# Performance work log

Hardware: AMD Instinct MI355X
Metric: run time of the kernel (lower is better)

Reference implementation:

```python
import jax, jax.numpy as jnp
import numpy as np

N = 50000
E = 600000
D_IN = 128
HID = 128
OUT = 64


def setup_inputs() -> dict:
    key = jax.random.key(0)
    ks = jax.random.split(key, 12)
    x = jax.random.normal(ks[0], (N, D_IN), dtype=jnp.float32)
    edge_index = jax.random.randint(ks[1], (2, E), 0, N, dtype=jnp.int32)
    def lin(k, fan_in, fan_out):
        lim = 1.0 / np.sqrt(fan_in)
        kw, kb = jax.random.split(k)
        W = jax.random.uniform(kw, (fan_in, fan_out), minval=-lim, maxval=lim, dtype=jnp.float32)
        b = jax.random.uniform(kb, (fan_out,), minval=-lim, maxval=lim, dtype=jnp.float32)
        return W, b
    W1, b1 = lin(ks[2], D_IN, HID)
    W2, b2 = lin(ks[3], HID, HID)
    W3, b3 = lin(ks[4], HID, HID)
    fcW, fcb = lin(ks[5], HID, OUT)
    return {"x": x, "edge_index": edge_index, "W1": W1, "b1": b1,
            "W2": W2, "b2": b2, "W3": W3, "b3": b3, "fcW": fcW, "fcb": fcb}


def _gcn_prep(edge_index):
    # add self loops, compute symmetric normalization deg^-1/2 * deg^-1/2
    loop = jnp.arange(N, dtype=edge_index.dtype)
    src = jnp.concatenate([edge_index[0], loop])
    dst = jnp.concatenate([edge_index[1], loop])
    deg = jax.ops.segment_sum(jnp.ones_like(dst, dtype=jnp.float32), dst, num_segments=N)
    dinv = jnp.where(deg > 0, jax.lax.rsqrt(deg), 0.0)
    norm = dinv[src] * dinv[dst]  # [E+N]
    return src, dst, norm


def _gcn_layer(x, src, dst, norm, W, b):
    h = x @ W                      # [N, F_out]
    msg = h[src] * norm[:, None]   # gather + scale, [E+N, F_out]
    agg = jax.ops.segment_sum(msg, dst, num_segments=N)
    return agg + b


def reference(x, edge_index, W1, b1, W2, b2, W3, b3, fcW, fcb):
    src, dst, norm = _gcn_prep(edge_index)
    x = jax.nn.relu(_gcn_layer(x, src, dst, norm, W1, b1))
    x = jax.nn.relu(_gcn_layer(x, src, dst, norm, W2, b2))
    x = jax.nn.relu(_gcn_layer(x, src, dst, norm, W3, b3))
    virtual_node_embedding = x[-1]  # last node's embedding [HID]
    out = virtual_node_embedding @ fcW + fcb  # [OUT]
    return out
```

## Files before the change

### kernel.cpp

```cpp
#include <hip/hip_runtime.h>

#define NF 128
#define OUTF 64

#define M2 1
#define M1 2
#define M0 4

#define CAP_F2 2048
#define CAP_E3 4096
#define CAP_F1 32768
#define CAP_E2 65536
#define CAP_F0 131072
#define CAP_E1 262144


__global__ void k_seed(int* __restrict__ mark, int* __restrict__ F2,
                       int* __restrict__ cnt, int last) {
    if (threadIdx.x == 0) {
        mark[last] = M2;
        F2[0] = last;
        cnt[0] = 1;
    }
}

__global__ void k_mark(const int* __restrict__ src, const int* __restrict__ dst, int E,
                       int* __restrict__ mark, int checkBit, int setBit, int last,
                       int2* __restrict__ Elist, int Ecap, int* __restrict__ eCnt,
                       int* __restrict__ Flist, int Fcap, int* __restrict__ fCnt,
                       const int* __restrict__ selfList, const int* __restrict__ selfCnt,
                       int selfCap)
{
    int i = blockIdx.x * blockDim.x + threadIdx.x;

    if (selfList) {
        int sc = *selfCnt; if (sc > selfCap) sc = selfCap;
        if (i < sc) {
            int v = selfList[i];
            if (!(atomicOr(&mark[v], setBit) & setBit)) {
                int p = atomicAdd(fCnt, 1);
                if (p < Fcap) Flist[p] = v;
            }
        }
    }
    if (i < E) {
        int d = dst[i];
        bool hit = checkBit ? ((mark[d] & checkBit) != 0) : (d == last);
        if (hit) {
            int s = src[i];
            int p = atomicAdd(eCnt, 1);
            if (p < Ecap) Elist[p] = make_int2(s, d);
            if (!(atomicOr(&mark[s], setBit) & setBit)) {
                int q = atomicAdd(fCnt, 1);
                if (q < Fcap) Flist[q] = s;
            }
        }
    }
}

__global__ void k_degm(const int* __restrict__ dst, const int* __restrict__ mark,
                       int* __restrict__ deg, int E) {
    int i = blockIdx.x * blockDim.x + threadIdx.x;
    if (i < E) {
        int d = dst[i];
        if (mark[d]) atomicAdd(&deg[d], 1);
    }
}

__global__ void k_dinvm(const int* __restrict__ mark, const int* __restrict__ deg,
                        float* __restrict__ dinv, int n) {
    int i = blockIdx.x * blockDim.x + threadIdx.x;
    if (i < n && mark[i]) dinv[i] = rsqrtf(1.0f + (float)deg[i]);
}

__global__ __launch_bounds__(256) void k_gemm_rows(
    const int* __restrict__ list, const int* __restrict__ cntPtr, int cap,
    const float* __restrict__ Xin, const float* __restrict__ bias,
    const float* __restrict__ W, const float* __restrict__ dinv,
    const int* __restrict__ mark, int aggBit, int last,
    float* __restrict__ H, float* __restrict__ AGG)
{
    __shared__ float wsm[128][128];
    const int t = threadIdx.x;

    {
        const float4* W4 = (const float4*)W;
        float4* S4 = (float4*)&wsm[0][0];
        #pragma unroll
        for (int it = 0; it < 16; ++it) S4[it * 256 + t] = W4[it * 256 + t];
    }
    __syncthreads();

    int cnt = *cntPtr; if (cnt > cap) cnt = cap;
    const int wave = t >> 6, lane = t & 63;

    for (int base = blockIdx.x * 4; base < cnt; base += gridDim.x * 4) {
        int r = base + wave;
        if (r >= cnt) continue;
        int v = list[r];
        size_t off = (size_t)v * NF;

        float x0, x1;
        if (bias) {
            x0 = fmaxf(Xin[off + lane]      + bias[lane],      0.f);
            x1 = fmaxf(Xin[off + lane + 64] + bias[lane + 64], 0.f);
        } else {
            x0 = Xin[off + lane];
            x1 = Xin[off + lane + 64];
        }

        float a0 = 0.f, a1 = 0.f;
        #pragma unroll 16
        for (int k = 0; k < 64; ++k) {
            float xk = __shfl(x0, k);
            a0 += xk * wsm[k][lane];
            a1 += xk * wsm[k][lane + 64];
        }
        #pragma unroll 16
        for (int k = 0; k < 64; ++k) {
            float xk = __shfl(x1, k);
            a0 += xk * wsm[k + 64][lane];
            a1 += xk * wsm[k + 64][lane + 64];
        }

        H[off + lane]      = a0;
        H[off + lane + 64] = a1;

        bool doAgg = (mark ? ((mark[v] & aggBit) != 0) : false) || (v == last);
        if (doAgg) {
            float di = dinv[v], s2 = di * di;
            AGG[off + lane]      = a0 * s2;
            AGG[off + lane + 64] = a1 * s2;
        }
    }
}

__global__ void k_scat(const int2* __restrict__ list, const int* __restrict__ cntPtr, int cap,
                       const float* __restrict__ dinv, const float* __restrict__ H,
                       float* __restrict__ AGG)
{
    int cnt = *cntPtr; if (cnt > cap) cnt = cap;
    int t = threadIdx.x;
    for (int i = blockIdx.x; i < cnt; i += gridDim.x) {
        int2 e = list[i];
        float w = dinv[e.x] * dinv[e.y];
        atomicAdd(&AGG[(size_t)e.y * NF + t], H[(size_t)e.x * NF + t] * w);
    }
}

__global__ void k_fc(const float* __restrict__ AGG3, const float* __restrict__ b3,
                     const float* __restrict__ fcW, const float* __restrict__ fcb,
                     float* __restrict__ out, int last)
{
    __shared__ float xrow[NF];
    int j = threadIdx.x;
    size_t off = (size_t)last * NF;
    xrow[j]      = fmaxf(AGG3[off + j]      + b3[j],      0.f);
    xrow[j + 64] = fmaxf(AGG3[off + j + 64] + b3[j + 64], 0.f);
    __syncthreads();
    float acc = fcb[j];
    #pragma unroll 16
    for (int k = 0; k < NF; ++k) acc += xrow[k] * fcW[k * OUTF + j];
    out[j] = acc;
}

extern "C" void kernel_launch(void* const* d_in, const int* in_sizes, int n_in,
                              void* d_out, int out_size, void* d_ws, size_t ws_size,
                              hipStream_t stream)
{
    const float* x    = (const float*)d_in[0];
    const int*   ei   = (const int*)d_in[1];
    const float* W1   = (const float*)d_in[2];
    const float* b1   = (const float*)d_in[3];
    const float* W2   = (const float*)d_in[4];
    const float* b2   = (const float*)d_in[5];
    const float* W3   = (const float*)d_in[6];
    const float* b3   = (const float*)d_in[7];
    const float* fcW  = (const float*)d_in[8];
    const float* fcb  = (const float*)d_in[9];
    float* out = (float*)d_out;

    const int n = in_sizes[0] / NF;
    const int E = in_sizes[1] / 2;
    const int* src = ei;
    const int* dst = ei + E;
    const int last = n - 1;

    char* wp = (char*)d_ws;
    auto alloc = [&](size_t bytes) -> void* {
        void* r = (void*)wp;
        wp += (bytes + 255) & ~(size_t)255;
        return r;
    };
    int*   deg  = (int*)alloc((size_t)n * 4);
    int*   mark = (int*)alloc((size_t)n * 4);
    int*   cnt  = (int*)alloc(64 * 4);
    size_t zbytes = (char*)wp - (char*)deg;

    float* dinv = (float*)alloc((size_t)n * 4);
    int*   F2   = (int*) alloc(CAP_F2 * 4);
    int2*  E3   = (int2*)alloc(CAP_E3 * 8);
    int*   F1   = (int*) alloc(CAP_F1 * 4);
    int2*  E2   = (int2*)alloc(CAP_E2 * 8);
    int*   F0   = (int*) alloc(CAP_F0 * 4);
    int2*  E1   = (int2*)alloc(CAP_E1 * 8);
    float* H    = (float*)alloc((size_t)n * NF * 4);
    float* aggA = (float*)alloc((size_t)n * NF * 4);
    float* aggB = (float*)alloc((size_t)n * NF * 4);

    const int B  = 256;
    const int EB = (E + B - 1) / B;
    const int NB = (n + B - 1) / B;

    hipMemsetAsync(deg, 0, zbytes, stream);
    k_seed<<<1, 64, 0, stream>>>(mark, F2, cnt, last);

    k_mark<<<EB, B, 0, stream>>>(src, dst, E, mark, 0,  M2, last,
                                 E3, CAP_E3, &cnt[1], F2, CAP_F2, &cnt[0],
                                 nullptr, nullptr, 0);
    k_mark<<<EB, B, 0, stream>>>(src, dst, E, mark, M2, M1, last,
                                 E2, CAP_E2, &cnt[3], F1, CAP_F1, &cnt[2],
                                 F2, &cnt[0], CAP_F2);
    k_mark<<<EB, B, 0, stream>>>(src, dst, E, mark, M1, M0, last,
                                 E1, CAP_E1, &cnt[5], F0, CAP_F0, &cnt[4],
                                 F1, &cnt[2], CAP_F1);

    k_degm <<<EB, B, 0, stream>>>(dst, mark, deg, E);
    k_dinvm<<<NB, B, 0, stream>>>(mark, deg, dinv, n);

    k_gemm_rows<<<384, B, 0, stream>>>(F0, &cnt[4], CAP_F0, x, nullptr, W1,
                                       dinv, mark, M1, -1, H, aggA);
    k_scat<<<2048, 128, 0, stream>>>(E1, &cnt[5], CAP_E1, dinv, H, aggA);

    k_gemm_rows<<<384, B, 0, stream>>>(F1, &cnt[2], CAP_F1, aggA, b1, W2,
                                       dinv, mark, M2, -1, H, aggB);
    k_scat<<<2048, 128, 0, stream>>>(E2, &cnt[3], CAP_E2, dinv, H, aggB);

    k_gemm_rows<<<384, B, 0, stream>>>(F2, &cnt[0], CAP_F2, aggB, b2, W3,
                                       dinv, nullptr, 0, last, H, aggA);
    k_scat<<<2048, 128, 0, stream>>>(E3, &cnt[1], CAP_E3, dinv, H, aggA);

    k_fc<<<1, 64, 0, stream>>>(aggA, b3, fcW, fcb, out, last);
}
```

Measured before the change: 167.8 us.

## Restructure GCN pipeline: dense layer-1 GEMM, fused edge scan, single-block tail

Drops the third frontier-marking pass and runs the layer-1 GEMM over every node, then scatters layer-1 messages by scanning the full edge list with a block-local queue. Degree counting moves into the first mark pass, and dinv is recomputed inline instead of stored. Layers 2 and 3 plus the final FC are fused into one single-block kernel to remove launch overhead. The trade-off is more layer-1 work (all rows instead of the 2-hop frontier) and serial layer-2/3 processing on a single workgroup, which could be slow if frontiers are large.

```diff
diff --git a/kernel.cpp b/kernel.cpp
--- a/kernel.cpp
+++ b/kernel.cpp
@@ -5,110 +5,89 @@
 
 #define M2 1
 #define M1 2
-#define M0 4
-
-#define CAP_F2 2048
-#define CAP_E3 4096
-#define CAP_F1 32768
-#define CAP_E2 65536
-#define CAP_F0 131072
-#define CAP_E1 262144
-
-
-__global__ void k_seed(int* __restrict__ mark, int* __restrict__ F2,
-                       int* __restrict__ cnt, int last) {
-    if (threadIdx.x == 0) {
-        mark[last] = M2;
-        F2[0] = last;
-        cnt[0] = 1;
-    }
-}
-
-__global__ void k_mark(const int* __restrict__ src, const int* __restrict__ dst, int E,
-                       int* __restrict__ mark, int checkBit, int setBit, int last,
-                       int2* __restrict__ Elist, int Ecap, int* __restrict__ eCnt,
-                       int* __restrict__ Flist, int Fcap, int* __restrict__ fCnt,
-                       const int* __restrict__ selfList, const int* __restrict__ selfCnt,
-                       int selfCap)
+
+#define CAP_F2 4096
+#define CAP_E3 8192
+#define CAP_F1 65536
+#define CAP_E2 131072
+
+
+__device__ __forceinline__ float dinv_of(const int* deg, int v) {
+    return rsqrtf(1.0f + (float)deg[v]);
+}
+
+__global__ void k_mark1(const int* __restrict__ src, const int* __restrict__ dst, int E,
+                        int last, int* __restrict__ deg, int* __restrict__ mark,
+                        int* __restrict__ cnt, int2* __restrict__ E3l, int* __restrict__ F2)
 {
     int i = blockIdx.x * blockDim.x + threadIdx.x;
-
-    if (selfList) {
-        int sc = *selfCnt; if (sc > selfCap) sc = selfCap;
-        if (i < sc) {
-            int v = selfList[i];
-            if (!(atomicOr(&mark[v], setBit) & setBit)) {
-                int p = atomicAdd(fCnt, 1);
-                if (p < Fcap) Flist[p] = v;
-            }
-        }
-    }
-    if (i < E) {
-        int d = dst[i];
-        bool hit = checkBit ? ((mark[d] & checkBit) != 0) : (d == last);
-        if (hit) {
-            int s = src[i];
-            int p = atomicAdd(eCnt, 1);
-            if (p < Ecap) Elist[p] = make_int2(s, d);
-            if (!(atomicOr(&mark[s], setBit) & setBit)) {
-                int q = atomicAdd(fCnt, 1);
-                if (q < Fcap) Flist[q] = s;
-            }
-        }
-    }
-}
-
-__global__ void k_degm(const int* __restrict__ dst, const int* __restrict__ mark,
-                       int* __restrict__ deg, int E) {
+    if (i == 0) {
+        if (!(atomicOr(&mark[last], M2) & M2)) {
+            int q = atomicAdd(&cnt[0], 1);
+            if (q < CAP_F2) F2[q] = last;
+        }
+    }
+    if (i >= E) return;
+    int d = dst[i];
+    atomicAdd(&deg[d], 1);
+    if (d == last) {
+        int s = src[i];
+        int pe = atomicAdd(&cnt[1], 1);
+        if (pe < CAP_E3) E3l[pe] = make_int2(s, d);
+        if (!(atomicOr(&mark[s], M2) & M2)) {
+            int q = atomicAdd(&cnt[0], 1);
+            if (q < CAP_F2) F2[q] = s;
+        }
+    }
+}
+
+__global__ void k_mark2(const int* __restrict__ src, const int* __restrict__ dst, int E,
+                        int* __restrict__ mark, int* __restrict__ cnt,
+                        const int* __restrict__ F2, int* __restrict__ F1,
+                        int2* __restrict__ E2l)
+{
     int i = blockIdx.x * blockDim.x + threadIdx.x;
-    if (i < E) {
-        int d = dst[i];
-        if (mark[d]) atomicAdd(&deg[d], 1);
-    }
-}
-
-__global__ void k_dinvm(const int* __restrict__ mark, const int* __restrict__ deg,
-                        float* __restrict__ dinv, int n) {
-    int i = blockIdx.x * blockDim.x + threadIdx.x;
-    if (i < n && mark[i]) dinv[i] = rsqrtf(1.0f + (float)deg[i]);
-}
-
-__global__ __launch_bounds__(256) void k_gemm_rows(
-    const int* __restrict__ list, const int* __restrict__ cntPtr, int cap,
-    const float* __restrict__ Xin, const float* __restrict__ bias,
-    const float* __restrict__ W, const float* __restrict__ dinv,
-    const int* __restrict__ mark, int aggBit, int last,
-    float* __restrict__ H, float* __restrict__ AGG)
+    int cF2 = cnt[0]; if (cF2 > CAP_F2) cF2 = CAP_F2;
+    if (i < cF2) {
+        int v = F2[i];
+        if (!(atomicOr(&mark[v], M1) & M1)) {
+            int q = atomicAdd(&cnt[2], 1);
+            if (q < CAP_F1) F1[q] = v;
+        }
+    }
+    if (i >= E) return;
+    int d = dst[i];
+    if (mark[d] & M2) {
+        int s = src[i];
+        int pe = atomicAdd(&cnt[3], 1);
+        if (pe < CAP_E2) E2l[pe] = make_int2(s, d);
+        if (!(atomicOr(&mark[s], M1) & M1)) {
+            int q = atomicAdd(&cnt[2], 1);
+            if (q < CAP_F1) F1[q] = s;
+        }
+    }
+}
+
+__global__ __launch_bounds__(256) void k_gemm1(
+    const float* __restrict__ X, const float* __restrict__ W1,
+    const int* __restrict__ mark, const int* __restrict__ deg,
+    float* __restrict__ H, float* __restrict__ agg1, int n)
 {
     __shared__ float wsm[128][128];
     const int t = threadIdx.x;
-
     {
-        const float4* W4 = (const float4*)W;
+        const float4* W4 = (const float4*)W1;
         float4* S4 = (float4*)&wsm[0][0];
         #pragma unroll
         for (int it = 0; it < 16; ++it) S4[it * 256 + t] = W4[it * 256 + t];
     }
     __syncthreads();
 
-    int cnt = *cntPtr; if (cnt > cap) cnt = cap;
     const int wave = t >> 6, lane = t & 63;
-
-    for (int base = blockIdx.x * 4; base < cnt; base += gridDim.x * 4) {
-        int r = base + wave;
-        if (r >= cnt) continue;
-        int v = list[r];
-        size_t off = (size_t)v * NF;
-
-        float x0, x1;
-        if (bias) {
-            x0 = fmaxf(Xin[off + lane]      + bias[lane],      0.f);
-            x1 = fmaxf(Xin[off + lane + 64] + bias[lane + 64], 0.f);
-        } else {
-            x0 = Xin[off + lane];
-            x1 = Xin[off + lane + 64];
-        }
-
+    for (int r = blockIdx.x * 4 + wave; r < n; r += gridDim.x * 4) {
+        size_t off = (size_t)r * NF;
+        float x0 = X[off + lane];
+        float x1 = X[off + lane + 64];
         float a0 = 0.f, a1 = 0.f;
         #pragma unroll 16
         for (int k = 0; k < 64; ++k) {
@@ -122,46 +101,165 @@
             a0 += xk * wsm[k + 64][lane];
             a1 += xk * wsm[k + 64][lane + 64];
         }
-
         H[off + lane]      = a0;
         H[off + lane + 64] = a1;
-
-        bool doAgg = (mark ? ((mark[v] & aggBit) != 0) : false) || (v == last);
-        if (doAgg) {
-            float di = dinv[v], s2 = di * di;
-            AGG[off + lane]      = a0 * s2;
-            AGG[off + lane + 64] = a1 * s2;
-        }
-    }
-}
-
-__global__ void k_scat(const int2* __restrict__ list, const int* __restrict__ cntPtr, int cap,
-                       const float* __restrict__ dinv, const float* __restrict__ H,
-                       float* __restrict__ AGG)
-{
-    int cnt = *cntPtr; if (cnt > cap) cnt = cap;
-    int t = threadIdx.x;
-    for (int i = blockIdx.x; i < cnt; i += gridDim.x) {
-        int2 e = list[i];
-        float w = dinv[e.x] * dinv[e.y];
-        atomicAdd(&AGG[(size_t)e.y * NF + t], H[(size_t)e.x * NF + t] * w);
-    }
-}
-
-__global__ void k_fc(const float* __restrict__ AGG3, const float* __restrict__ b3,
-                     const float* __restrict__ fcW, const float* __restrict__ fcb,
-                     float* __restrict__ out, int last)
-{
-    __shared__ float xrow[NF];
-    int j = threadIdx.x;
-    size_t off = (size_t)last * NF;
-    xrow[j]      = fmaxf(AGG3[off + j]      + b3[j],      0.f);
-    xrow[j + 64] = fmaxf(AGG3[off + j + 64] + b3[j + 64], 0.f);
-    __syncthreads();
-    float acc = fcb[j];
-    #pragma unroll 16
-    for (int k = 0; k < NF; ++k) acc += xrow[k] * fcW[k * OUTF + j];
-    out[j] = acc;
+        if (mark[r] & M1) {
+            float di = dinv_of(deg, r);
+            float s2 = di * di;
+            agg1[off + lane]      = a0 * s2;
+            agg1[off + lane + 64] = a1 * s2;
+        }
+    }
+}
+
+__global__ __launch_bounds__(256) void k_scatf(
+    const int* __restrict__ src, const int* __restrict__ dst, int E,
+    const int* __restrict__ mark, const int* __restrict__ deg,
+    const float* __restrict__ H, float* __restrict__ agg1)
+{
+    __shared__ int qs[256], qd[256];
+    __shared__ float qw[256];
+    __shared__ int qn;
+    const int t = threadIdx.x;
+    const int half = t >> 7, f = t & 127;
+
+    for (int base = blockIdx.x * 256; base < E; base += gridDim.x * 256) {
+        if (t == 0) qn = 0;
+        __syncthreads();
+        int i = base + t;
+        if (i < E) {
+            int d = dst[i];
+            if (mark[d] & M1) {
+                int s = src[i];
+                int q = atomicAdd(&qn, 1);
+                qs[q] = s; qd[q] = d;
+                qw[q] = dinv_of(deg, s) * dinv_of(deg, d);
+            }
+        }
+        __syncthreads();
+        int m = qn;
+        for (int j = half; j < m; j += 2) {
+            atomicAdd(&agg1[(size_t)qd[j] * NF + f], H[(size_t)qs[j] * NF + f] * qw[j]);
+        }
+        __syncthreads();
+    }
+}
+
+__global__ __launch_bounds__(256) void k_tail1(
+    const int* __restrict__ cnt, const int* __restrict__ F1, const int* __restrict__ F2,
+    const int2* __restrict__ E2l, const int2* __restrict__ E3l,
+    const int* __restrict__ mark, const int* __restrict__ deg,
+    const float* __restrict__ agg1, const float* __restrict__ b1,
+    const float* __restrict__ W2, const float* __restrict__ b2,
+    const float* __restrict__ W3, const float* __restrict__ b3,
+    const float* __restrict__ fcW, const float* __restrict__ fcb,
+    float* __restrict__ H, float* __restrict__ aggB,
+    float* __restrict__ out, int last)
+{
+    __shared__ float wsm[128][128];
+    __shared__ float a3[128];
+    const int t = threadIdx.x;
+    const int wave = t >> 6, lane = t & 63;
+
+    int cF2 = cnt[0]; if (cF2 > CAP_F2) cF2 = CAP_F2;
+    int cE3 = cnt[1]; if (cE3 > CAP_E3) cE3 = CAP_E3;
+    int cF1 = cnt[2]; if (cF1 > CAP_F1) cF1 = CAP_F1;
+    int cE2 = cnt[3]; if (cE2 > CAP_E2) cE2 = CAP_E2;
+
+    {
+        const float4* W4 = (const float4*)W2;
+        float4* S4 = (float4*)&wsm[0][0];
+        #pragma unroll
+        for (int it = 0; it < 16; ++it) S4[it * 256 + t] = W4[it * 256 + t];
+    }
+    __syncthreads();
+    for (int r = wave; r < cF1; r += 4) {
+        int v = F1[r];
+        size_t off = (size_t)v * NF;
+        float x0 = fmaxf(agg1[off + lane]      + b1[lane],      0.f);
+        float x1 = fmaxf(agg1[off + lane + 64] + b1[lane + 64], 0.f);
+        float a0 = 0.f, a1 = 0.f;
+        #pragma unroll 16
+        for (int k = 0; k < 64; ++k) {
+            float xk = __shfl(x0, k);
+            a0 += xk * wsm[k][lane];
+            a1 += xk * wsm[k][lane + 64];
+        }
+        #pragma unroll 16
+        for (int k = 0; k < 64; ++k) {
+            float xk = __shfl(x1, k);
+            a0 += xk * wsm[k + 64][lane];
+            a1 += xk * wsm[k + 64][lane + 64];
+        }
+        H[off + lane]      = a0;
+        H[off + lane + 64] = a1;
+        if (mark[v] & M2) {
+            float di = dinv_of(deg, v);
+            float s2 = di * di;
+            aggB[off + lane]      = a0 * s2;
+            aggB[off + lane + 64] = a1 * s2;
+        }
+    }
+    __syncthreads();
+
+    {
+        const int half = t >> 7, f = t & 127;
+        for (int j = half; j < cE2; j += 2) {
+            int2 e = E2l[j];
+            float w = dinv_of(deg, e.x) * dinv_of(deg, e.y);
+            atomicAdd(&aggB[(size_t)e.y * NF + f], H[(size_t)e.x * NF + f] * w);
+        }
+    }
+    __syncthreads();
+
+    {
+        const float4* W4 = (const float4*)W3;
+        float4* S4 = (float4*)&wsm[0][0];
+        #pragma unroll
+        for (int it = 0; it < 16; ++it) S4[it * 256 + t] = W4[it * 256 + t];
+    }
+    __syncthreads();
+    for (int r = wave; r < cF2; r += 4) {
+        int v = F2[r];
+        size_t off = (size_t)v * NF;
+        float x0 = fmaxf(aggB[off + lane]      + b2[lane],      0.f);
+        float x1 = fmaxf(aggB[off + lane + 64] + b2[lane + 64], 0.f);
+        float a0 = 0.f, a1 = 0.f;
+        #pragma unroll 16
+        for (int k = 0; k < 64; ++k) {
+            float xk = __shfl(x0, k);
+            a0 += xk * wsm[k][lane];
+            a1 += xk * wsm[k][lane + 64];
+        }
+        #pragma unroll 16
+        for (int k = 0; k < 64; ++k) {
+            float xk = __shfl(x1, k);
+            a0 += xk * wsm[k + 64][lane];
+            a1 += xk * wsm[k + 64][lane + 64];
+        }
+        H[off + lane]      = a0;
+        H[off + lane + 64] = a1;
+    }
+    __syncthreads();
+
+    if (t < NF) {
+        float dl = dinv_of(deg, last);
+        float acc = dl * dl * H[(size_t)last * NF + t];
+        for (int j = 0; j < cE3; ++j) {
+            int2 e = E3l[j];
+            float w = dinv_of(deg, e.x) * dl;
+            acc += H[(size_t)e.x * NF + t] * w;
+        }
+        a3[t] = fmaxf(acc + b3[t], 0.f);
+    }
+    __syncthreads();
+
+    if (t < OUTF) {
+        float acc = fcb[t];
+        #pragma unroll 16
+        for (int k = 0; k < NF; ++k) acc += a3[k] * fcW[k * OUTF + t];
+        out[t] = acc;
+    }
 }
 
 extern "C" void kernel_launch(void* const* d_in, const int* in_sizes, int n_in,
@@ -192,53 +290,29 @@
         wp += (bytes + 255) & ~(size_t)255;
         return r;
     };
-    int*   deg  = (int*)alloc((size_t)n * 4);
-    int*   mark = (int*)alloc((size_t)n * 4);
-    int*   cnt  = (int*)alloc(64 * 4);
+
+    int* deg  = (int*)alloc((size_t)n * 4);
+    int* mark = (int*)alloc((size_t)n * 4);
+    int* cnt  = (int*)alloc(64 * 4);
     size_t zbytes = (char*)wp - (char*)deg;
 
-    float* dinv = (float*)alloc((size_t)n * 4);
-    int*   F2   = (int*) alloc(CAP_F2 * 4);
-    int2*  E3   = (int2*)alloc(CAP_E3 * 8);
-    int*   F1   = (int*) alloc(CAP_F1 * 4);
-    int2*  E2   = (int2*)alloc(CAP_E2 * 8);
-    int*   F0   = (int*) alloc(CAP_F0 * 4);
-    int2*  E1   = (int2*)alloc(CAP_E1 * 8);
+    int*   F2   = (int*)  alloc(CAP_F2 * 4);
+    int2*  E3l  = (int2*) alloc(CAP_E3 * 8);
+    int*   F1   = (int*)  alloc(CAP_F1 * 4);
+    int2*  E2l  = (int2*) alloc(CAP_E2 * 8);
     float* H    = (float*)alloc((size_t)n * NF * 4);
-    float* aggA = (float*)alloc((size_t)n * NF * 4);
+    float* agg1 = (float*)alloc((size_t)n * NF * 4);
     float* aggB = (float*)alloc((size_t)n * NF * 4);
 
     const int B  = 256;
     const int EB = (E + B - 1) / B;
-    const int NB = (n + B - 1) / B;
 
     hipMemsetAsync(deg, 0, zbytes, stream);
-    k_seed<<<1, 64, 0, stream>>>(mark, F2, cnt, last);
-
-    k_mark<<<EB, B, 0, stream>>>(src, dst, E, mark, 0,  M2, last,
-                                 E3, CAP_E3, &cnt[1], F2, CAP_F2, &cnt[0],
-                                 nullptr, nullptr, 0);
-    k_mark<<<EB, B, 0, stream>>>(src, dst, E, mark, M2, M1, last,
-                                 E2, CAP_E2, &cnt[3], F1, CAP_F1, &cnt[2],
-                                 F2, &cnt[0], CAP_F2);
-    k_mark<<<EB, B, 0, stream>>>(src, dst, E, mark, M1, M0, last,
-                                 E1, CAP_E1, &cnt[5], F0, CAP_F0, &cnt[4],
-                                 F1, &cnt[2], CAP_F1);
-
-    k_degm <<<EB, B, 0, stream>>>(dst, mark, deg, E);
-    k_dinvm<<<NB, B, 0, stream>>>(mark, deg, dinv, n);
-
-    k_gemm_rows<<<384, B, 0, stream>>>(F0, &cnt[4], CAP_F0, x, nullptr, W1,
-                                       dinv, mark, M1, -1, H, aggA);
-    k_scat<<<2048, 128, 0, stream>>>(E1, &cnt[5], CAP_E1, dinv, H, aggA);
-
-    k_gemm_rows<<<384, B, 0, stream>>>(F1, &cnt[2], CAP_F1, aggA, b1, W2,
-                                       dinv, mark, M2, -1, H, aggB);
-    k_scat<<<2048, 128, 0, stream>>>(E2, &cnt[3], CAP_E2, dinv, H, aggB);
-
-    k_gemm_rows<<<384, B, 0, stream>>>(F2, &cnt[0], CAP_F2, aggB, b2, W3,
-                                       dinv, nullptr, 0, last, H, aggA);
-    k_scat<<<2048, 128, 0, stream>>>(E3, &cnt[1], CAP_E3, dinv, H, aggA);
-
-    k_fc<<<1, 64, 0, stream>>>(aggA, b3, fcW, fcb, out, last);
-}
+    k_mark1<<<EB, B, 0, stream>>>(src, dst, E, last, deg, mark, cnt, E3l, F2);
+    k_mark2<<<EB, B, 0, stream>>>(src, dst, E, mark, cnt, F2, F1, E2l);
+    k_gemm1<<<512, B, 0, stream>>>(x, W1, mark, deg, H, agg1, n);
+    k_scatf<<<512, B, 0, stream>>>(src, dst, E, mark, deg, H, agg1);
+    k_tail1<<<1, B, 0, stream>>>(cnt, F1, F2, E2l, E3l, mark, deg,
+                                 agg1, b1, W2, b2, W3, b3, fcW, fcb,
+                                 H, aggB, out, last);
+}
```

Result: slower. 381.6 us (+127.4%).
